# Kernel tuning notes

Hardware: AMD Instinct MI355X
Metric: run time of the kernel (lower is better)

## Reference

```python
import jax, jax.numpy as jnp
import numpy as np

NUM_HEADS = 16  # from init_kwargs


def setup_inputs() -> dict:
    key = jax.random.key(0)
    k1, k2, k3, k4, k5 = jax.random.split(key, 5)
    B, N, C = 2, 2048, 1024
    return {
        "query": jax.random.normal(k1, (B, N, C), dtype=jnp.float32),
        "key": jax.random.normal(k2, (B, N, C), dtype=jnp.float32),
        "value": jax.random.normal(k3, (B, N, C), dtype=jnp.float32),
        "W_merge": jax.random.normal(k4, (C, C), dtype=jnp.float32) * (1.0 / np.sqrt(C)),
        "b_merge": jax.random.normal(k5, (C,), dtype=jnp.float32) * 0.02,
    }


def reference(query, key, value, W_merge, b_merge):
    B, N, C = query.shape
    H = NUM_HEADS
    dim = C // H
    # Faithful to torch: plain reshape (B,N,C) -> (B, dim, H, N), no transpose.
    q = query.reshape(B, dim, H, -1)
    k = key.reshape(B, dim, H, -1)
    v = value.reshape(B, dim, H, -1)
    # Faithful scale: divide by sqrt(N) (sequence length), as in the source.
    scale = 1.0 / np.sqrt(N).astype(np.float32)
    scores = jnp.einsum('bdhn,bdhm->bhnm', q, k) * scale  # [B,H,N,N]
    attn = jax.nn.softmax(scores, axis=-1)
    x = jnp.einsum('bhnm,bdhm->bdhn', attn, v)  # [B,dim,H,N]
    x = x.reshape(B, C, -1)  # [B,C,N]
    # Conv1d(C,C,kernel_size=1) == pointwise channel matmul + bias
    out = jnp.einsum('oc,bcn->bon', W_merge, x) + b_merge[None, :, None]
    return out  # [B,C,N]
```

## Files before the change

### kernel.cpp

```cpp
#include <hip/hip_runtime.h>


#define H 16
#define NSEQ 2048
#define CCH 1024
#define BATCH 2
#define DSTR (H * NSEQ)

typedef __attribute__((ext_vector_type(8))) short bf16x8;
typedef __attribute__((ext_vector_type(4))) float f32x4;
typedef __attribute__((ext_vector_type(16))) float f32x16;
typedef __attribute__((ext_vector_type(4))) unsigned int uint32x4;

__device__ __forceinline__ unsigned short f2bf(float x) {
  unsigned int u = __builtin_bit_cast(unsigned int, x);
  u += 0x7FFFu + ((u >> 16) & 1u);
  return (unsigned short)(u >> 16);
}

__device__ __forceinline__ unsigned int pack2bf(float a, float b) {
#if __has_builtin(__builtin_amdgcn_cvt_pk_bf16_f32)
  typedef __attribute__((ext_vector_type(2))) __bf16 bf16x2_t;
  bf16x2_t r = __builtin_amdgcn_cvt_pk_bf16_f32(a, b);
  return __builtin_bit_cast(unsigned int, r);
#else
  unsigned int ua = __builtin_bit_cast(unsigned int, a);
  unsigned int ub = __builtin_bit_cast(unsigned int, b);
  ua += 0x7FFFu + ((ua >> 16) & 1u);
  ub += 0x7FFFu + ((ub >> 16) & 1u);
  return __builtin_amdgcn_perm(ub, ua, 0x07060302u);
#endif
}

__device__ __forceinline__ float fast_exp2(float x) {
#if __has_builtin(__builtin_amdgcn_exp2f)
  return __builtin_amdgcn_exp2f(x);
#else
  return exp2f(x);
#endif
}

__device__ __forceinline__ void permswap32(unsigned int& a, unsigned int& b) {
#if __has_builtin(__builtin_amdgcn_permlane32_swap)
  typedef __attribute__((ext_vector_type(2))) unsigned int uint2v;
  uint2v r = __builtin_amdgcn_permlane32_swap(a, b, false, false);
  a = r[0];
  b = r[1];
#else
  unsigned int ax = (unsigned int)__shfl_xor((int)a, 32, 64);
  unsigned int bx = (unsigned int)__shfl_xor((int)b, 32, 64);
  bool lo = (threadIdx.x & 63) < 32;
  unsigned int na = lo ? a : bx;
  unsigned int nb = lo ? ax : b;
  a = na;
  b = nb;
#endif
}

__device__ __forceinline__ void gld16(const void* g, void* l) {
  __builtin_amdgcn_global_load_lds(
      (const __attribute__((address_space(1))) unsigned int*)g,
      (__attribute__((address_space(3))) unsigned int*)l, 16, 0, 0);
}

__device__ __forceinline__ f32x16 zero16() {
  f32x16 v;
#pragma unroll
  for (int i = 0; i < 16; ++i) v[i] = 0.f;
  return v;
}

__global__ __launch_bounds__(256) void prep_all(const float* __restrict__ W,
                                                const float* __restrict__ v,
                                                const float* __restrict__ q,
                                                const float* __restrict__ k,
                                                unsigned short* __restrict__ Wp,
                                                unsigned short* __restrict__ Vb,
                                                unsigned short* __restrict__ Qt,
                                                unsigned short* __restrict__ Kt) {
  __shared__ unsigned short T[64][72];
  const int bid = blockIdx.x, tid = threadIdx.x;

  if (bid < 1024) {
    const int o = bid;
    const int cp = tid * 4;
    const int hh = cp >> 6;
    const int d0 = cp & 63;
    const float* Wr = W + (size_t)o * CCH;
    ushort4 ov;
    ov.x = f2bf(Wr[(d0 + 0) * H + hh]);
    ov.y = f2bf(Wr[(d0 + 1) * H + hh]);
    ov.z = f2bf(Wr[(d0 + 2) * H + hh]);
    ov.w = f2bf(Wr[(d0 + 3) * H + hh]);
    *(ushort4*)&Wp[(size_t)o * CCH + cp] = ov;
  } else if (bid < 5120) {
    int idx = (bid - 1024) * 256 + tid;
    float4 x = ((const float4*)v)[idx];
    ushort4 o;
    o.x = f2bf(x.x); o.y = f2bf(x.y); o.z = f2bf(x.z); o.w = f2bf(x.w);
    ((ushort4*)Vb)[idx] = o;
  } else {
    const int lbid = bid - 5120;
    const int n0 = (lbid & 31) * 64;
    const int hh = (lbid >> 5) & 15;
    const int zz = lbid >> 9;
    const int b = zz >> 1, t = zz & 1;
    const float* src = t ? k : q;
    unsigned short* dst = t ? Kt : Qt;
    const float scl = t ? 1.0f : (0.022097086912079608f * 1.4426950408889634f);
    const size_t base = (size_t)b * (CCH * NSEQ) + (size_t)hh * NSEQ;
#pragma unroll
    for (int it = 0; it < 4; ++it) {
      int i4 = it * 256 + tid;
      int d = i4 >> 4;
      int nn = (i4 & 15) << 2;
      float4 val = *(const float4*)(src + base + (size_t)d * DSTR + n0 + nn);
      T[nn + 0][d] = f2bf(val.x * scl);
      T[nn + 1][d] = f2bf(val.y * scl);
      T[nn + 2][d] = f2bf(val.z * scl);
      T[nn + 3][d] = f2bf(val.w * scl);
    }
    __syncthreads();
    const size_t obase = ((size_t)(b * H + hh) * NSEQ + n0) * 64;
#pragma unroll
    for (int it = 0; it < 2; ++it) {
      int idx = it * 256 + tid;
      int row = idx >> 3, cb = idx & 7;
      *(bf16x8*)(dst + obase + (size_t)row * 64 + cb * 8) = *(const bf16x8*)&T[row][cb * 8];
    }
  }
}

__global__ __launch_bounds__(512, 4) void attn6(const unsigned short* __restrict__ Qt,
                                                const unsigned short* __restrict__ Kt,
                                                const unsigned short* __restrict__ Vb,
                                                unsigned short* __restrict__ xt) {
  __shared__ __align__(16) unsigned char sbuf[65536 + 1024];
  unsigned short* KV = (unsigned short*)sbuf;
  float* lsumLDS = (float*)(sbuf + 65536);
  float* Oex = (float*)sbuf;

  const int tid = threadIdx.x;
  const int w = tid >> 6, lane = tid & 63;
  const int lane31 = lane & 31, hl = lane >> 5;
  const int g = w >> 2, nw = w & 3;
  const int n0 = blockIdx.x * 128;
  const int hh = blockIdx.y, b = blockIdx.z;

  const unsigned short* Qbase = Qt + ((size_t)(b * H + hh) * NSEQ + n0) * 64;
  const unsigned short* Kg = Kt + ((size_t)(b * H + hh) * NSEQ + g * 1024) * 64;
  const unsigned short* Vg = Vb + (size_t)b * (CCH * NSEQ) + (size_t)hh * NSEQ + g * 1024;

  const int r8 = lane >> 3, scb = lane & 7;

#define KVOFF(gg, bb, kk) ((((gg)*2 + (bb)) * 2 + (kk)) * 4096)

#pragma unroll
  for (int i = 0; i < 2; ++i) {
    int row = i * 64 + w * 8 + r8;
    int cbl = scb ^ (row & 7);
    gld16(Qbase + (size_t)row * 64 + cbl * 8, KV + (i * 64 + w * 8) * 64);
  }
  __syncthreads();

  bf16x8 bQ[4];
#pragma unroll
  for (int ks = 0; ks < 4; ++ks) {
    int row = nw * 32 + lane31;
    int phys = (ks * 2 + hl) ^ (row & 7);
    bQ[ks] = *(const bf16x8*)(KV + (size_t)row * 64 + phys * 8);
  }
  __syncthreads();

#pragma unroll
  for (int i = 0; i < 2; ++i) {
    int row = i * 32 + nw * 8 + r8;
    int cbl = scb ^ (row & 7);
    gld16(Kg + (size_t)row * 64 + cbl * 8, KV + KVOFF(g, 0, 0) + (i * 32 + nw * 8) * 64);
    gld16(Vg + (size_t)row * DSTR + cbl * 8, KV + KVOFF(g, 0, 1) + (i * 32 + nw * 8) * 64);
  }
  __syncthreads();

  f32x16 O[2];
  O[0] = zero16();
  O[1] = zero16();
  float lsum = 0.f;

  for (int it = 0; it < 16; ++it) {
    const int cur = it & 1;
    if (it < 15) {
      const int nxt = cur ^ 1;
      const int m0n = (it + 1) * 64;
#pragma unroll
      for (int i = 0; i < 2; ++i) {
        int row = i * 32 + nw * 8 + r8;
        int cbl = scb ^ (row & 7);
        gld16(Kg + (size_t)(m0n + row) * 64 + cbl * 8,
              KV + KVOFF(g, nxt, 0) + (i * 32 + nw * 8) * 64);
        gld16(Vg + (size_t)row * DSTR + m0n + cbl * 8,
              KV + KVOFF(g, nxt, 1) + (i * 32 + nw * 8) * 64);
      }
    }

#pragma unroll
    for (int mt = 0; mt < 2; ++mt) {
      f32x16 St = zero16();
#pragma unroll
      for (int ks = 0; ks < 4; ++ks) {
        int row = mt * 32 + lane31;
        int phys = (ks * 2 + hl) ^ (row & 7);
        bf16x8 aK = *(const bf16x8*)(KV + KVOFF(g, cur, 0) + row * 64 + phys * 8);
        St = __builtin_amdgcn_mfma_f32_32x32x16_bf16(aK, bQ[ks], St, 0, 0, 0);
      }

      unsigned int pd[8];
#pragma unroll
      for (int t = 0; t < 8; ++t) {
        float e0 = fast_exp2(St[2 * t]);
        float e1 = fast_exp2(St[2 * t + 1]);
        lsum += e0 + e1;
        pd[t] = pack2bf(e0, e1);
      }

      unsigned int s0[4] = {pd[0], pd[1], pd[2], pd[3]};
      unsigned int s1[4] = {pd[4], pd[5], pd[6], pd[7]};
      permswap32(s0[0], s0[2]);
      permswap32(s0[1], s0[3]);
      permswap32(s1[0], s1[2]);
      permswap32(s1[1], s1[3]);

#pragma unroll
      for (int ms = 0; ms < 2; ++ms) {
        bf16x8 bV[2];
#pragma unroll
        for (int dt = 0; dt < 2; ++dt) {
          int row = dt * 32 + lane31;
          int phys = (mt * 4 + ms * 2 + hl) ^ (row & 7);
          bV[dt] = *(const bf16x8*)(KV + KVOFF(g, cur, 1) + row * 64 + phys * 8);
        }
        const unsigned int* sp = ms ? s1 : s0;
        bf16x8 aP = __builtin_bit_cast(bf16x8, (uint32x4){sp[0], sp[1], sp[2], sp[3]});
        O[0] = __builtin_amdgcn_mfma_f32_32x32x16_bf16(aP, bV[0], O[0], 0, 0, 0);
        O[1] = __builtin_amdgcn_mfma_f32_32x32x16_bf16(aP, bV[1], O[1], 0, 0, 0);
      }
    }
    __syncthreads();
  }

  lsum += __shfl_xor(lsum, 32, 64);
  if (hl == 0) lsumLDS[g * 128 + nw * 32 + lane31] = lsum;
  if (g == 1) {
#pragma unroll
    for (int dt = 0; dt < 2; ++dt)
#pragma unroll
      for (int r = 0; r < 16; ++r) {
        int nl = nw * 32 + (r & 3) + 8 * (r >> 2) + 4 * hl;
        Oex[nl * 64 + dt * 32 + lane31] = O[dt][r];
      }
  }
  __syncthreads();
  if (g == 0) {
    const size_t xb = (size_t)b * ((size_t)NSEQ * CCH);
#pragma unroll
    for (int rq = 0; rq < 4; ++rq) {
      int nlb = nw * 32 + rq * 8 + 4 * hl;
      float4 l0 = *(const float4*)&lsumLDS[nlb];
      float4 l1 = *(const float4*)&lsumLDS[128 + nlb];
      float inv0 = 1.0f / (l0.x + l1.x);
      float inv1 = 1.0f / (l0.y + l1.y);
      float inv2 = 1.0f / (l0.z + l1.z);
      float inv3 = 1.0f / (l0.w + l1.w);
#pragma unroll
      for (int dt = 0; dt < 2; ++dt) {
        int d = dt * 32 + lane31;
#pragma unroll
        for (int rr = 0; rr < 4; ++rr) {
          int r = rq * 4 + rr;
          float val = O[dt][r] + Oex[(nlb + rr) * 64 + d];
          float inv = (rr == 0) ? inv0 : (rr == 1) ? inv1 : (rr == 2) ? inv2 : inv3;
          int n = n0 + nlb + rr;
          xt[xb + (size_t)n * CCH + hh * 64 + d] = f2bf(val * inv);
        }
      }
    }
  }
#undef KVOFF
}

__global__ __launch_bounds__(256) void merge5(const unsigned short* __restrict__ Wp,
                                              const unsigned short* __restrict__ xt,
                                              const float* __restrict__ bias,
                                              float* __restrict__ out) {
  __shared__ unsigned short At[2][64 * 64];
  __shared__ unsigned short Bt[2][64 * 64];
  const int tid = threadIdx.x;
  const int w = tid >> 6, lane = tid & 63;
  const int quad = lane >> 4, l16 = lane & 15;
  const int wx = w & 1, wy = w >> 1;
  const int n0 = blockIdx.x * 64, o0 = blockIdx.y * 64, b = blockIdx.z;
  const int srow = w * 8 + (lane >> 3), scb = lane & 7;
  const unsigned short* Bbase = xt + (size_t)b * ((size_t)NSEQ * CCH);

  f32x4 acc[2][2];
#pragma unroll
  for (int ot = 0; ot < 2; ++ot)
#pragma unroll
    for (int nt = 0; nt < 2; ++nt) acc[ot][nt] = (f32x4){0.f, 0.f, 0.f, 0.f};

#pragma unroll
  for (int i = 0; i < 2; ++i) {
    int row = i * 32 + srow;
    int cbl = scb ^ (row & 7);
    gld16(Wp + (size_t)(o0 + row) * CCH + cbl * 8, &At[0][(i * 32 + w * 8) * 64]);
    gld16(Bbase + (size_t)(n0 + row) * CCH + cbl * 8, &Bt[0][(i * 32 + w * 8) * 64]);
  }
  __syncthreads();

  for (int it = 0; it < 16; ++it) {
    const int cur = it & 1;
    if (it < 15) {
      const int nxt = cur ^ 1;
      const int c0 = (it + 1) * 64;
#pragma unroll
      for (int i = 0; i < 2; ++i) {
        int row = i * 32 + srow;
        int cbl = scb ^ (row & 7);
        gld16(Wp + (size_t)(o0 + row) * CCH + c0 + cbl * 8, &At[nxt][(i * 32 + w * 8) * 64]);
        gld16(Bbase + (size_t)(n0 + row) * CCH + c0 + cbl * 8, &Bt[nxt][(i * 32 + w * 8) * 64]);
      }
    }
#pragma unroll
    for (int ks = 0; ks < 2; ++ks) {
      int phys = ((ks * 4 + quad) ^ (l16 & 7)) * 8;
      bf16x8 aW[2], bX[2];
#pragma unroll
      for (int ot = 0; ot < 2; ++ot)
        aW[ot] = *(const bf16x8*)&At[cur][(wy * 32 + ot * 16 + l16) * 64 + phys];
#pragma unroll
      for (int nt = 0; nt < 2; ++nt)
        bX[nt] = *(const bf16x8*)&Bt[cur][(wx * 32 + nt * 16 + l16) * 64 + phys];
#pragma unroll
      for (int ot = 0; ot < 2; ++ot)
#pragma unroll
        for (int nt = 0; nt < 2; ++nt)
          acc[ot][nt] =
              __builtin_amdgcn_mfma_f32_16x16x32_bf16(aW[ot], bX[nt], acc[ot][nt], 0, 0, 0);
    }
    __syncthreads();
  }

#pragma unroll
  for (int ot = 0; ot < 2; ++ot) {
#pragma unroll
    for (int r = 0; r < 4; ++r) {
      int o = o0 + wy * 32 + ot * 16 + quad * 4 + r;
      float br = bias[o];
#pragma unroll
      for (int nt = 0; nt < 2; ++nt)
        out[(size_t)b * ((size_t)CCH * NSEQ) + (size_t)o * NSEQ + n0 + wx * 32 + nt * 16 + l16] =
            acc[ot][nt][r] + br;
    }
  }
}

extern "C" void kernel_launch(void* const* d_in, const int* in_sizes, int n_in,
                              void* d_out, int out_size, void* d_ws, size_t ws_size,
                              hipStream_t stream) {
  const float* q = (const float*)d_in[0];
  const float* k = (const float*)d_in[1];
  const float* v = (const float*)d_in[2];
  const float* W = (const float*)d_in[3];
  const float* bias = (const float*)d_in[4];
  float* out = (float*)d_out;

  unsigned short* Wp = (unsigned short*)d_ws;
  unsigned short* xt = Wp + (1u << 20);
  unsigned short* Qt = xt + (4u << 20);
  unsigned short* Kt = Qt + (4u << 20);
  unsigned short* Vb = Kt + (4u << 20);

  hipLaunchKernelGGL(prep_all, dim3(7168), dim3(256), 0, stream, W, v, q, k, Wp, Vb, Qt, Kt);
  hipLaunchKernelGGL(attn6, dim3(NSEQ / 128, H, BATCH), dim3(512), 0, stream, Qt, Kt, Vb, xt);
  hipLaunchKernelGGL(merge5, dim3(NSEQ / 64, CCH / 64, BATCH), dim3(256), 0, stream,
                     Wp, xt, bias, out);
}
```

Before: 162.4 us.

## Software-pipeline QK MFMA ahead of softmax and change LDS swizzle

Restructures the attention inner loop so the QK^T tile for the next sub-block is issued before the exp/pack and PV MFMAs of the current one. This includes computing the first tile of the next iteration right after the barrier. The goal is to overlap MFMA latency with the VALU exp work. It also widens the LDS XOR swizzle to mix in row bits 3-4, reducing bank conflicts, and splits the row-sum into two accumulators to shorten the dependency chain. An extra live f32x16 accumulator raises register pressure, which could hurt occupancy.

```diff
diff --git a/kernel.cpp b/kernel.cpp
--- a/kernel.cpp
+++ b/kernel.cpp
@@ -8,6 +8,7 @@
 #define DSTR (H * NSEQ)
 
 typedef __attribute__((ext_vector_type(8))) short bf16x8;
+typedef __attribute__((ext_vector_type(2))) float f32x2;
 typedef __attribute__((ext_vector_type(4))) float f32x4;
 typedef __attribute__((ext_vector_type(16))) float f32x16;
 typedef __attribute__((ext_vector_type(4))) unsigned int uint32x4;
@@ -69,6 +70,8 @@
   for (int i = 0; i < 16; ++i) v[i] = 0.f;
   return v;
 }
+
+__device__ __forceinline__ int swzr(int row) { return (row & 7) ^ ((row >> 3) & 3); }
 
 __global__ __launch_bounds__(256) void prep_all(const float* __restrict__ W,
                                                 const float* __restrict__ v,
@@ -131,7 +134,60 @@
   }
 }
 
-__global__ __launch_bounds__(512, 4) void attn6(const unsigned short* __restrict__ Qt,
+
+__device__ __forceinline__ f32x16 qk_tile(const unsigned short* Kt, int mt, int lane31,
+                                          int hl, const bf16x8* bQ) {
+  const int row = mt * 32 + lane31;
+  const int s = swzr(row);
+  const unsigned short* rp = Kt + (size_t)row * 64;
+  f32x16 St = zero16();
+#pragma unroll
+  for (int ks = 0; ks < 4; ++ks) {
+    bf16x8 aK = *(const bf16x8*)(rp + (((ks * 2 + hl) ^ s) * 8));
+    St = __builtin_amdgcn_mfma_f32_32x32x16_bf16(aK, bQ[ks], St, 0, 0, 0);
+  }
+  return St;
+}
+
+__device__ __forceinline__ void exppack(const f32x16& St, f32x2& ls2, bf16x8& a0, bf16x8& a1) {
+  unsigned int pd[8];
+#pragma unroll
+  for (int t = 0; t < 8; ++t) {
+    float e0 = fast_exp2(St[2 * t]);
+    float e1 = fast_exp2(St[2 * t + 1]);
+    ls2 += (f32x2){e0, e1};
+    pd[t] = pack2bf(e0, e1);
+  }
+  unsigned int s0[4] = {pd[0], pd[1], pd[2], pd[3]};
+  unsigned int s1[4] = {pd[4], pd[5], pd[6], pd[7]};
+  permswap32(s0[0], s0[2]);
+  permswap32(s0[1], s0[3]);
+  permswap32(s1[0], s1[2]);
+  permswap32(s1[1], s1[3]);
+  a0 = __builtin_bit_cast(bf16x8, (uint32x4){s0[0], s0[1], s0[2], s0[3]});
+  a1 = __builtin_bit_cast(bf16x8, (uint32x4){s1[0], s1[1], s1[2], s1[3]});
+}
+
+__device__ __forceinline__ void pv_tile(const unsigned short* Vt, int mt, bf16x8 a0, bf16x8 a1,
+                                        int lane31, int hl, f32x16& O0, f32x16& O1) {
+#pragma unroll
+  for (int ms = 0; ms < 2; ++ms) {
+    bf16x8 bV0, bV1;
+    {
+      int row = lane31;
+      bV0 = *(const bf16x8*)(Vt + (size_t)row * 64 + (((mt * 4 + ms * 2 + hl) ^ swzr(row)) * 8));
+    }
+    {
+      int row = 32 + lane31;
+      bV1 = *(const bf16x8*)(Vt + (size_t)row * 64 + (((mt * 4 + ms * 2 + hl) ^ swzr(row)) * 8));
+    }
+    bf16x8 aP = ms ? a1 : a0;
+    O0 = __builtin_amdgcn_mfma_f32_32x32x16_bf16(aP, bV0, O0, 0, 0, 0);
+    O1 = __builtin_amdgcn_mfma_f32_32x32x16_bf16(aP, bV1, O1, 0, 0, 0);
+  }
+}
+
+__global__ __launch_bounds__(512, 4) void attn7(const unsigned short* __restrict__ Qt,
                                                 const unsigned short* __restrict__ Kt,
                                                 const unsigned short* __restrict__ Vb,
                                                 unsigned short* __restrict__ xt) {
@@ -158,7 +214,7 @@
 #pragma unroll
   for (int i = 0; i < 2; ++i) {
     int row = i * 64 + w * 8 + r8;
-    int cbl = scb ^ (row & 7);
+    int cbl = scb ^ swzr(row);
     gld16(Qbase + (size_t)row * 64 + cbl * 8, KV + (i * 64 + w * 8) * 64);
   }
   __syncthreads();
@@ -167,7 +223,7 @@
 #pragma unroll
   for (int ks = 0; ks < 4; ++ks) {
     int row = nw * 32 + lane31;
-    int phys = (ks * 2 + hl) ^ (row & 7);
+    int phys = (ks * 2 + hl) ^ swzr(row);
     bQ[ks] = *(const bf16x8*)(KV + (size_t)row * 64 + phys * 8);
   }
   __syncthreads();
@@ -175,7 +231,7 @@
 #pragma unroll
   for (int i = 0; i < 2; ++i) {
     int row = i * 32 + nw * 8 + r8;
-    int cbl = scb ^ (row & 7);
+    int cbl = scb ^ swzr(row);
     gld16(Kg + (size_t)row * 64 + cbl * 8, KV + KVOFF(g, 0, 0) + (i * 32 + nw * 8) * 64);
     gld16(Vg + (size_t)row * DSTR + cbl * 8, KV + KVOFF(g, 0, 1) + (i * 32 + nw * 8) * 64);
   }
@@ -184,7 +240,9 @@
   f32x16 O[2];
   O[0] = zero16();
   O[1] = zero16();
-  float lsum = 0.f;
+  f32x2 ls2 = {0.f, 0.f};
+
+  f32x16 St0 = qk_tile(KV + KVOFF(g, 0, 0), 0, lane31, hl, bQ);
 
   for (int it = 0; it < 16; ++it) {
     const int cur = it & 1;
@@ -194,7 +252,7 @@
 #pragma unroll
       for (int i = 0; i < 2; ++i) {
         int row = i * 32 + nw * 8 + r8;
-        int cbl = scb ^ (row & 7);
+        int cbl = scb ^ swzr(row);
         gld16(Kg + (size_t)(m0n + row) * 64 + cbl * 8,
               KV + KVOFF(g, nxt, 0) + (i * 32 + nw * 8) * 64);
         gld16(Vg + (size_t)row * DSTR + m0n + cbl * 8,
@@ -202,51 +260,23 @@
       }
     }
 
-#pragma unroll
-    for (int mt = 0; mt < 2; ++mt) {
-      f32x16 St = zero16();
-#pragma unroll
-      for (int ks = 0; ks < 4; ++ks) {
-        int row = mt * 32 + lane31;
-        int phys = (ks * 2 + hl) ^ (row & 7);
-        bf16x8 aK = *(const bf16x8*)(KV + KVOFF(g, cur, 0) + row * 64 + phys * 8);
-        St = __builtin_amdgcn_mfma_f32_32x32x16_bf16(aK, bQ[ks], St, 0, 0, 0);
-      }
-
-      unsigned int pd[8];
-#pragma unroll
-      for (int t = 0; t < 8; ++t) {
-        float e0 = fast_exp2(St[2 * t]);
-        float e1 = fast_exp2(St[2 * t + 1]);
-        lsum += e0 + e1;
-        pd[t] = pack2bf(e0, e1);
-      }
-
-      unsigned int s0[4] = {pd[0], pd[1], pd[2], pd[3]};
-      unsigned int s1[4] = {pd[4], pd[5], pd[6], pd[7]};
-      permswap32(s0[0], s0[2]);
-      permswap32(s0[1], s0[3]);
-      permswap32(s1[0], s1[2]);
-      permswap32(s1[1], s1[3]);
-
-#pragma unroll
-      for (int ms = 0; ms < 2; ++ms) {
-        bf16x8 bV[2];
-#pragma unroll
-        for (int dt = 0; dt < 2; ++dt) {
-          int row = dt * 32 + lane31;
-          int phys = (mt * 4 + ms * 2 + hl) ^ (row & 7);
-          bV[dt] = *(const bf16x8*)(KV + KVOFF(g, cur, 1) + row * 64 + phys * 8);
-        }
-        const unsigned int* sp = ms ? s1 : s0;
-        bf16x8 aP = __builtin_bit_cast(bf16x8, (uint32x4){sp[0], sp[1], sp[2], sp[3]});
-        O[0] = __builtin_amdgcn_mfma_f32_32x32x16_bf16(aP, bV[0], O[0], 0, 0, 0);
-        O[1] = __builtin_amdgcn_mfma_f32_32x32x16_bf16(aP, bV[1], O[1], 0, 0, 0);
-      }
-    }
+    const unsigned short* Ktile = KV + KVOFF(g, cur, 0);
+    const unsigned short* Vtile = KV + KVOFF(g, cur, 1);
+
+    f32x16 St1 = qk_tile(Ktile, 1, lane31, hl, bQ);
+
+    bf16x8 a0, a1;
+    exppack(St0, ls2, a0, a1);
+    pv_tile(Vtile, 0, a0, a1, lane31, hl, O[0], O[1]);
+
+    exppack(St1, ls2, a0, a1);
+    pv_tile(Vtile, 1, a0, a1, lane31, hl, O[0], O[1]);
+
     __syncthreads();
-  }
-
+    if (it < 15) St0 = qk_tile(KV + KVOFF(g, cur ^ 1, 0), 0, lane31, hl, bQ);
+  }
+
+  float lsum = ls2[0] + ls2[1];
   lsum += __shfl_xor(lsum, 32, 64);
   if (hl == 0) lsumLDS[g * 128 + nw * 32 + lane31] = lsum;
   if (g == 1) {
@@ -380,7 +410,7 @@
   unsigned short* Vb = Kt + (4u << 20);
 
   hipLaunchKernelGGL(prep_all, dim3(7168), dim3(256), 0, stream, W, v, q, k, Wp, Vb, Qt, Kt);
-  hipLaunchKernelGGL(attn6, dim3(NSEQ / 128, H, BATCH), dim3(512), 0, stream, Qt, Kt, Vb, xt);
+  hipLaunchKernelGGL(attn7, dim3(NSEQ / 128, H, BATCH), dim3(512), 0, stream, Qt, Kt, Vb, xt);
   hipLaunchKernelGGL(merge5, dim3(NSEQ / 64, CCH / 64, BATCH), dim3(256), 0, stream,
                      Wp, xt, bias, out);
 }
```

Result: no change. 162.8 us (+0.3%).

## Restructure attention inner loop with unrolled double buffering, precomputed LDS pointers, and setprio

Applied to the files above, without the earlier changes.

Rewrites the attention kernel's main loop into a manually unrolled two-stage ping-pong, with LDS read pointers and global staging pointers precomputed outside the loop. It also changes the LDS swizzle to XOR in extra row bits, to reduce bank conflicts. MFMA sections are bracketed with s_setprio so matrix work gets issue priority over the exp and pack work, and the row sum is kept as a two-wide vector to shorten the dependency chain. The aim is to cut address arithmetic and conflicts and to improve overlap. The cost is more complex code and possible register pressure, and the new swizzle has to stay consistent with the layout used in the epilogue.

```diff
diff --git a/kernel.cpp b/kernel.cpp
--- a/kernel.cpp
+++ b/kernel.cpp
@@ -8,6 +8,7 @@
 #define DSTR (H * NSEQ)
 
 typedef __attribute__((ext_vector_type(8))) short bf16x8;
+typedef __attribute__((ext_vector_type(2))) float f32x2;
 typedef __attribute__((ext_vector_type(4))) float f32x4;
 typedef __attribute__((ext_vector_type(16))) float f32x16;
 typedef __attribute__((ext_vector_type(4))) unsigned int uint32x4;
@@ -69,6 +70,8 @@
   for (int i = 0; i < 16; ++i) v[i] = 0.f;
   return v;
 }
+
+__device__ __forceinline__ int swzr(int row) { return (row & 7) ^ ((row >> 3) & 3); }
 
 __global__ __launch_bounds__(256) void prep_all(const float* __restrict__ W,
                                                 const float* __restrict__ v,
@@ -131,7 +134,37 @@
   }
 }
 
-__global__ __launch_bounds__(512, 4) void attn6(const unsigned short* __restrict__ Qt,
+
+__device__ __forceinline__ f32x16 qk4(const char* const* kp, int off, const bf16x8* bQ) {
+  f32x16 St = zero16();
+#pragma unroll
+  for (int ks = 0; ks < 4; ++ks) {
+    bf16x8 aK = *(const bf16x8*)(kp[ks] + off);
+    St = __builtin_amdgcn_mfma_f32_32x32x16_bf16(aK, bQ[ks], St, 0, 0, 0);
+  }
+  return St;
+}
+
+__device__ __forceinline__ void exppack(const f32x16& St, f32x2& ls2, bf16x8& a0, bf16x8& a1) {
+  unsigned int pd[8];
+#pragma unroll
+  for (int t = 0; t < 8; ++t) {
+    float e0 = fast_exp2(St[2 * t]);
+    float e1 = fast_exp2(St[2 * t + 1]);
+    ls2 += (f32x2){e0, e1};
+    pd[t] = pack2bf(e0, e1);
+  }
+  unsigned int s0[4] = {pd[0], pd[1], pd[2], pd[3]};
+  unsigned int s1[4] = {pd[4], pd[5], pd[6], pd[7]};
+  permswap32(s0[0], s0[2]);
+  permswap32(s0[1], s0[3]);
+  permswap32(s1[0], s1[2]);
+  permswap32(s1[1], s1[3]);
+  a0 = __builtin_bit_cast(bf16x8, (uint32x4){s0[0], s0[1], s0[2], s0[3]});
+  a1 = __builtin_bit_cast(bf16x8, (uint32x4){s1[0], s1[1], s1[2], s1[3]});
+}
+
+__global__ __launch_bounds__(512, 4) void attn8(const unsigned short* __restrict__ Qt,
                                                 const unsigned short* __restrict__ Kt,
                                                 const unsigned short* __restrict__ Vb,
                                                 unsigned short* __restrict__ xt) {
@@ -158,7 +191,7 @@
 #pragma unroll
   for (int i = 0; i < 2; ++i) {
     int row = i * 64 + w * 8 + r8;
-    int cbl = scb ^ (row & 7);
+    int cbl = scb ^ swzr(row);
     gld16(Qbase + (size_t)row * 64 + cbl * 8, KV + (i * 64 + w * 8) * 64);
   }
   __syncthreads();
@@ -167,86 +200,98 @@
 #pragma unroll
   for (int ks = 0; ks < 4; ++ks) {
     int row = nw * 32 + lane31;
-    int phys = (ks * 2 + hl) ^ (row & 7);
+    int phys = (ks * 2 + hl) ^ swzr(row);
     bQ[ks] = *(const bf16x8*)(KV + (size_t)row * 64 + phys * 8);
   }
   __syncthreads();
 
-#pragma unroll
-  for (int i = 0; i < 2; ++i) {
-    int row = i * 32 + nw * 8 + r8;
-    int cbl = scb ^ (row & 7);
-    gld16(Kg + (size_t)row * 64 + cbl * 8, KV + KVOFF(g, 0, 0) + (i * 32 + nw * 8) * 64);
-    gld16(Vg + (size_t)row * DSTR + cbl * 8, KV + KVOFF(g, 0, 1) + (i * 32 + nw * 8) * 64);
-  }
+  const char* KVc = (const char*)KV;
+  const int sz = swzr(lane31);
+  const char* kp[4];
+#pragma unroll
+  for (int ks = 0; ks < 4; ++ks)
+    kp[ks] = KVc + g * 32768 + lane31 * 128 + (((ks * 2 + hl) ^ sz) * 16);
+
+  const int srow0 = nw * 8 + r8;
+  const int cswz = (scb ^ swzr(srow0)) * 16;
+  const char* kgp0 = (const char*)Kg + (size_t)srow0 * 128 + cswz;
+  const char* kgp1 = kgp0 + 4096;
+  const char* vgp0 = (const char*)Vg + (size_t)srow0 * (DSTR * 2) + cswz;
+  const char* vgp1 = vgp0 + (size_t)32 * DSTR * 2;
+
+  unsigned short* ldsK0 = KV + KVOFF(g, 0, 0) + (nw * 8) * 64;
+  unsigned short* ldsK1 = ldsK0 + 32 * 64;
+  unsigned short* ldsV0 = KV + KVOFF(g, 0, 1) + (nw * 8) * 64;
+  unsigned short* ldsV1 = ldsV0 + 32 * 64;
+
+  gld16(kgp0, ldsK0);
+  gld16(kgp1, ldsK1);
+  gld16(vgp0, ldsV0);
+  gld16(vgp1, ldsV1);
+  kgp0 += 8192; kgp1 += 8192; vgp0 += 128; vgp1 += 128;
   __syncthreads();
 
   f32x16 O[2];
   O[0] = zero16();
   O[1] = zero16();
-  float lsum = 0.f;
-
-  for (int it = 0; it < 16; ++it) {
-    const int cur = it & 1;
-    if (it < 15) {
-      const int nxt = cur ^ 1;
-      const int m0n = (it + 1) * 64;
-#pragma unroll
-      for (int i = 0; i < 2; ++i) {
-        int row = i * 32 + nw * 8 + r8;
-        int cbl = scb ^ (row & 7);
-        gld16(Kg + (size_t)(m0n + row) * 64 + cbl * 8,
-              KV + KVOFF(g, nxt, 0) + (i * 32 + nw * 8) * 64);
-        gld16(Vg + (size_t)row * DSTR + m0n + cbl * 8,
-              KV + KVOFF(g, nxt, 1) + (i * 32 + nw * 8) * 64);
-      }
-    }
-
-#pragma unroll
-    for (int mt = 0; mt < 2; ++mt) {
-      f32x16 St = zero16();
-#pragma unroll
-      for (int ks = 0; ks < 4; ++ks) {
-        int row = mt * 32 + lane31;
-        int phys = (ks * 2 + hl) ^ (row & 7);
-        bf16x8 aK = *(const bf16x8*)(KV + KVOFF(g, cur, 0) + row * 64 + phys * 8);
-        St = __builtin_amdgcn_mfma_f32_32x32x16_bf16(aK, bQ[ks], St, 0, 0, 0);
-      }
-
-      unsigned int pd[8];
-#pragma unroll
-      for (int t = 0; t < 8; ++t) {
-        float e0 = fast_exp2(St[2 * t]);
-        float e1 = fast_exp2(St[2 * t + 1]);
-        lsum += e0 + e1;
-        pd[t] = pack2bf(e0, e1);
-      }
-
-      unsigned int s0[4] = {pd[0], pd[1], pd[2], pd[3]};
-      unsigned int s1[4] = {pd[4], pd[5], pd[6], pd[7]};
-      permswap32(s0[0], s0[2]);
-      permswap32(s0[1], s0[3]);
-      permswap32(s1[0], s1[2]);
-      permswap32(s1[1], s1[3]);
-
-#pragma unroll
-      for (int ms = 0; ms < 2; ++ms) {
-        bf16x8 bV[2];
-#pragma unroll
-        for (int dt = 0; dt < 2; ++dt) {
-          int row = dt * 32 + lane31;
-          int phys = (mt * 4 + ms * 2 + hl) ^ (row & 7);
-          bV[dt] = *(const bf16x8*)(KV + KVOFF(g, cur, 1) + row * 64 + phys * 8);
-        }
-        const unsigned int* sp = ms ? s1 : s0;
-        bf16x8 aP = __builtin_bit_cast(bf16x8, (uint32x4){sp[0], sp[1], sp[2], sp[3]});
-        O[0] = __builtin_amdgcn_mfma_f32_32x32x16_bf16(aP, bV[0], O[0], 0, 0, 0);
-        O[1] = __builtin_amdgcn_mfma_f32_32x32x16_bf16(aP, bV[1], O[1], 0, 0, 0);
-      }
-    }
-    __syncthreads();
-  }
-
+  f32x2 ls2 = {0.f, 0.f};
+
+#define VREAD(C, DT, CUR) (*(const bf16x8*)(kp[C] + 8192 + (DT)*4096 + (CUR)*16384))
+
+#define PVT(MT, CUR, A0, A1)                                                     \
+  {                                                                              \
+    bf16x8 v00 = VREAD((MT)*2 + 0, 0, CUR);                                      \
+    bf16x8 v01 = VREAD((MT)*2 + 0, 1, CUR);                                      \
+    bf16x8 v10 = VREAD((MT)*2 + 1, 0, CUR);                                      \
+    bf16x8 v11 = VREAD((MT)*2 + 1, 1, CUR);                                      \
+    O[0] = __builtin_amdgcn_mfma_f32_32x32x16_bf16(A0, v00, O[0], 0, 0, 0);      \
+    O[1] = __builtin_amdgcn_mfma_f32_32x32x16_bf16(A0, v01, O[1], 0, 0, 0);      \
+    O[0] = __builtin_amdgcn_mfma_f32_32x32x16_bf16(A1, v10, O[0], 0, 0, 0);      \
+    O[1] = __builtin_amdgcn_mfma_f32_32x32x16_bf16(A1, v11, O[1], 0, 0, 0);      \
+  }
+
+#define ATTN_ITER(CUR, DO_STAGE)                                                 \
+  {                                                                              \
+    if (DO_STAGE) {                                                              \
+      gld16(kgp0, ldsK0 + (1 - (CUR)) * 8192);                                   \
+      gld16(kgp1, ldsK1 + (1 - (CUR)) * 8192);                                   \
+      gld16(vgp0, ldsV0 + (1 - (CUR)) * 8192);                                   \
+      gld16(vgp1, ldsV1 + (1 - (CUR)) * 8192);                                   \
+      kgp0 += 8192; kgp1 += 8192; vgp0 += 128; vgp1 += 128;                      \
+    }                                                                            \
+    {                                                                            \
+      __builtin_amdgcn_s_setprio(1);                                             \
+      f32x16 St = qk4(kp, (CUR)*16384, bQ);                                      \
+      __builtin_amdgcn_s_setprio(0);                                             \
+      bf16x8 a0, a1;                                                             \
+      exppack(St, ls2, a0, a1);                                                  \
+      __builtin_amdgcn_s_setprio(1);                                             \
+      PVT(0, CUR, a0, a1);                                                       \
+      __builtin_amdgcn_s_setprio(0);                                             \
+    }                                                                            \
+    {                                                                            \
+      __builtin_amdgcn_s_setprio(1);                                             \
+      f32x16 St = qk4(kp, 4096 + (CUR)*16384, bQ);                               \
+      __builtin_amdgcn_s_setprio(0);                                             \
+      bf16x8 a0, a1;                                                             \
+      exppack(St, ls2, a0, a1);                                                  \
+      __builtin_amdgcn_s_setprio(1);                                             \
+      PVT(1, CUR, a0, a1);                                                       \
+      __builtin_amdgcn_s_setprio(0);                                             \
+    }                                                                            \
+    __syncthreads();                                                             \
+  }
+
+  for (int j = 0; j < 8; ++j) {
+    ATTN_ITER(0, 1);
+    ATTN_ITER(1, (j < 7));
+  }
+
+#undef ATTN_ITER
+#undef PVT
+#undef VREAD
+
+  float lsum = ls2[0] + ls2[1];
   lsum += __shfl_xor(lsum, 32, 64);
   if (hl == 0) lsumLDS[g * 128 + nw * 32 + lane31] = lsum;
   if (g == 1) {
@@ -380,7 +425,7 @@
   unsigned short* Vb = Kt + (4u << 20);
 
   hipLaunchKernelGGL(prep_all, dim3(7168), dim3(256), 0, stream, W, v, q, k, Wp, Vb, Qt, Kt);
-  hipLaunchKernelGGL(attn6, dim3(NSEQ / 128, H, BATCH), dim3(512), 0, stream, Qt, Kt, Vb, xt);
+  hipLaunchKernelGGL(attn8, dim3(NSEQ / 128, H, BATCH), dim3(512), 0, stream, Qt, Kt, Vb, xt);
   hipLaunchKernelGGL(merge5, dim3(NSEQ / 64, CCH / 64, BATCH), dim3(256), 0, stream,
                      Wp, xt, bias, out);
 }
```

Result: slower. 167.6 us (+3.2%).

## Pre-swizzle K and V into MFMA fragment order and load directly from global

Applied to the files above, without the earlier changes.

The prep kernel now writes K and V in a layout that matches the MFMA operand fragments, with V transposed through shared memory. The attention kernel then drops its LDS double buffering and per-tile block barriers, and loads K/V fragments straight from global memory with register double buffering. It also adds s_setprio around the MFMA groups. This removes LDS traffic and synchronisation, but relies on L2/cache hits for K/V reuse across waves and issues many small global loads.

```diff
diff --git a/kernel.cpp b/kernel.cpp
--- a/kernel.cpp
+++ b/kernel.cpp
@@ -8,6 +8,7 @@
 #define DSTR (H * NSEQ)
 
 typedef __attribute__((ext_vector_type(8))) short bf16x8;
+typedef __attribute__((ext_vector_type(2))) float f32x2;
 typedef __attribute__((ext_vector_type(4))) float f32x4;
 typedef __attribute__((ext_vector_type(16))) float f32x16;
 typedef __attribute__((ext_vector_type(4))) unsigned int uint32x4;
@@ -75,10 +76,11 @@
                                                 const float* __restrict__ q,
                                                 const float* __restrict__ k,
                                                 unsigned short* __restrict__ Wp,
-                                                unsigned short* __restrict__ Vb,
+                                                unsigned short* __restrict__ VB,
                                                 unsigned short* __restrict__ Qt,
-                                                unsigned short* __restrict__ Kt) {
+                                                unsigned short* __restrict__ KA) {
   __shared__ unsigned short T[64][72];
+  __shared__ unsigned short VL[256 * 8];
   const int bid = blockIdx.x, tid = threadIdx.x;
 
   if (bid < 1024) {
@@ -93,20 +95,29 @@
     ov.z = f2bf(Wr[(d0 + 2) * H + hh]);
     ov.w = f2bf(Wr[(d0 + 3) * H + hh]);
     *(ushort4*)&Wp[(size_t)o * CCH + cp] = ov;
-  } else if (bid < 5120) {
-    int idx = (bid - 1024) * 256 + tid;
-    float4 x = ((const float4*)v)[idx];
-    ushort4 o;
-    o.x = f2bf(x.x); o.y = f2bf(x.y); o.z = f2bf(x.z); o.w = f2bf(x.w);
-    ((ushort4*)Vb)[idx] = o;
+  } else if (bid < 3072) {
+    const int vb = bid - 1024;
+    const int bh = vb >> 6, kbb = vb & 63;
+    const int bb = bh >> 4, hhh = bh & 15;
+    const int d = tid >> 2, nq = (tid & 3) * 8;
+    const float* srcv =
+        v + (size_t)bb * (CCH * NSEQ) + (size_t)d * DSTR + hhh * NSEQ + kbb * 32 + nq;
+    float4 x0 = *(const float4*)srcv;
+    float4 x1 = *(const float4*)(srcv + 4);
+    unsigned short* Lc = &VL[tid * 8];
+    Lc[0] = f2bf(x0.x); Lc[1] = f2bf(x0.y); Lc[2] = f2bf(x0.z); Lc[3] = f2bf(x0.w);
+    Lc[4] = f2bf(x1.x); Lc[5] = f2bf(x1.y); Lc[6] = f2bf(x1.z); Lc[7] = f2bf(x1.w);
+    __syncthreads();
+    const int kb_lo = tid >> 6, d2 = tid & 63;
+    *(bf16x8*)(VB + (size_t)bh * 131072 + (size_t)(kbb * 4 + kb_lo) * 512 + d2 * 8) =
+        *(const bf16x8*)&VL[(d2 * 4 + kb_lo) * 8];
   } else {
-    const int lbid = bid - 5120;
+    const int lbid = bid - 3072;
     const int n0 = (lbid & 31) * 64;
     const int hh = (lbid >> 5) & 15;
     const int zz = lbid >> 9;
     const int b = zz >> 1, t = zz & 1;
     const float* src = t ? k : q;
-    unsigned short* dst = t ? Kt : Qt;
     const float scl = t ? 1.0f : (0.022097086912079608f * 1.4426950408889634f);
     const size_t base = (size_t)b * (CCH * NSEQ) + (size_t)hh * NSEQ;
 #pragma unroll
@@ -121,24 +132,54 @@
       T[nn + 3][d] = f2bf(val.w * scl);
     }
     __syncthreads();
-    const size_t obase = ((size_t)(b * H + hh) * NSEQ + n0) * 64;
-#pragma unroll
-    for (int it = 0; it < 2; ++it) {
-      int idx = it * 256 + tid;
-      int row = idx >> 3, cb = idx & 7;
-      *(bf16x8*)(dst + obase + (size_t)row * 64 + cb * 8) = *(const bf16x8*)&T[row][cb * 8];
-    }
-  }
-}
-
-__global__ __launch_bounds__(512, 4) void attn6(const unsigned short* __restrict__ Qt,
-                                                const unsigned short* __restrict__ Kt,
-                                                const unsigned short* __restrict__ Vb,
+    if (t == 0) {
+      const size_t obase = ((size_t)(b * H + hh) * NSEQ + n0) * 64;
+#pragma unroll
+      for (int it = 0; it < 2; ++it) {
+        int idx = it * 256 + tid;
+        int row = idx >> 3, cb = idx & 7;
+        *(bf16x8*)(Qt + obase + (size_t)row * 64 + cb * 8) = *(const bf16x8*)&T[row][cb * 8];
+      }
+    } else {
+      const size_t obase = (size_t)(b * H + hh) * 131072 + (size_t)(n0 >> 5) * 2048;
+#pragma unroll
+      for (int it = 0; it < 2; ++it) {
+        int idx = it * 256 + tid;
+        int nl = idx >> 3, sub = idx & 7;
+        *(bf16x8*)(KA + obase + (size_t)(nl >> 5) * 2048 + sub * 256 + (nl & 31) * 8) =
+            *(const bf16x8*)&T[nl][sub * 8];
+      }
+    }
+  }
+}
+
+
+__device__ __forceinline__ void exppack(const f32x16& St, f32x2& ls2, bf16x8& a0, bf16x8& a1) {
+  unsigned int pd[8];
+#pragma unroll
+  for (int t = 0; t < 8; ++t) {
+    float e0 = fast_exp2(St[2 * t]);
+    float e1 = fast_exp2(St[2 * t + 1]);
+    ls2 += (f32x2){e0, e1};
+    pd[t] = pack2bf(e0, e1);
+  }
+  unsigned int s0[4] = {pd[0], pd[1], pd[2], pd[3]};
+  unsigned int s1[4] = {pd[4], pd[5], pd[6], pd[7]};
+  permswap32(s0[0], s0[2]);
+  permswap32(s0[1], s0[3]);
+  permswap32(s1[0], s1[2]);
+  permswap32(s1[1], s1[3]);
+  a0 = __builtin_bit_cast(bf16x8, (uint32x4){s0[0], s0[1], s0[2], s0[3]});
+  a1 = __builtin_bit_cast(bf16x8, (uint32x4){s1[0], s1[1], s1[2], s1[3]});
+}
+
+__global__ __launch_bounds__(512, 4) void attn9(const unsigned short* __restrict__ Qt,
+                                                const unsigned short* __restrict__ KA,
+                                                const unsigned short* __restrict__ VB,
                                                 unsigned short* __restrict__ xt) {
-  __shared__ __align__(16) unsigned char sbuf[65536 + 1024];
-  unsigned short* KV = (unsigned short*)sbuf;
-  float* lsumLDS = (float*)(sbuf + 65536);
-  float* Oex = (float*)sbuf;
+  __shared__ __align__(16) float eplds[128 * 64 + 256];
+  float* Oex = eplds;
+  float* lsumLDS = eplds + 8192;
 
   const int tid = threadIdx.x;
   const int w = tid >> 6, lane = tid & 63;
@@ -146,107 +187,67 @@
   const int g = w >> 2, nw = w & 3;
   const int n0 = blockIdx.x * 128;
   const int hh = blockIdx.y, b = blockIdx.z;
-
-  const unsigned short* Qbase = Qt + ((size_t)(b * H + hh) * NSEQ + n0) * 64;
-  const unsigned short* Kg = Kt + ((size_t)(b * H + hh) * NSEQ + g * 1024) * 64;
-  const unsigned short* Vg = Vb + (size_t)b * (CCH * NSEQ) + (size_t)hh * NSEQ + g * 1024;
-
-  const int r8 = lane >> 3, scb = lane & 7;
-
-#define KVOFF(gg, bb, kk) ((((gg)*2 + (bb)) * 2 + (kk)) * 4096)
-
-#pragma unroll
-  for (int i = 0; i < 2; ++i) {
-    int row = i * 64 + w * 8 + r8;
-    int cbl = scb ^ (row & 7);
-    gld16(Qbase + (size_t)row * 64 + cbl * 8, KV + (i * 64 + w * 8) * 64);
-  }
-  __syncthreads();
+  const int bh = b * H + hh;
 
   bf16x8 bQ[4];
-#pragma unroll
-  for (int ks = 0; ks < 4; ++ks) {
-    int row = nw * 32 + lane31;
-    int phys = (ks * 2 + hl) ^ (row & 7);
-    bQ[ks] = *(const bf16x8*)(KV + (size_t)row * 64 + phys * 8);
-  }
-  __syncthreads();
-
-#pragma unroll
-  for (int i = 0; i < 2; ++i) {
-    int row = i * 32 + nw * 8 + r8;
-    int cbl = scb ^ (row & 7);
-    gld16(Kg + (size_t)row * 64 + cbl * 8, KV + KVOFF(g, 0, 0) + (i * 32 + nw * 8) * 64);
-    gld16(Vg + (size_t)row * DSTR + cbl * 8, KV + KVOFF(g, 0, 1) + (i * 32 + nw * 8) * 64);
-  }
-  __syncthreads();
+  const unsigned short* Qb = Qt + ((size_t)bh * NSEQ + n0 + nw * 32 + lane31) * 64;
+#pragma unroll
+  for (int ks = 0; ks < 4; ++ks) bQ[ks] = *(const bf16x8*)(Qb + (ks * 2 + hl) * 8);
+
+  const unsigned short* kp = KA + (size_t)bh * 131072 + g * 65536 + hl * 256 + lane31 * 8;
+  const unsigned short* vp = VB + (size_t)bh * 131072 + g * 65536 + hl * 512 + lane31 * 8;
 
   f32x16 O[2];
   O[0] = zero16();
   O[1] = zero16();
-  float lsum = 0.f;
-
-  for (int it = 0; it < 16; ++it) {
-    const int cur = it & 1;
-    if (it < 15) {
-      const int nxt = cur ^ 1;
-      const int m0n = (it + 1) * 64;
-#pragma unroll
-      for (int i = 0; i < 2; ++i) {
-        int row = i * 32 + nw * 8 + r8;
-        int cbl = scb ^ (row & 7);
-        gld16(Kg + (size_t)(m0n + row) * 64 + cbl * 8,
-              KV + KVOFF(g, nxt, 0) + (i * 32 + nw * 8) * 64);
-        gld16(Vg + (size_t)row * DSTR + m0n + cbl * 8,
-              KV + KVOFF(g, nxt, 1) + (i * 32 + nw * 8) * 64);
-      }
-    }
-
-#pragma unroll
-    for (int mt = 0; mt < 2; ++mt) {
-      f32x16 St = zero16();
-#pragma unroll
-      for (int ks = 0; ks < 4; ++ks) {
-        int row = mt * 32 + lane31;
-        int phys = (ks * 2 + hl) ^ (row & 7);
-        bf16x8 aK = *(const bf16x8*)(KV + KVOFF(g, cur, 0) + row * 64 + phys * 8);
-        St = __builtin_amdgcn_mfma_f32_32x32x16_bf16(aK, bQ[ks], St, 0, 0, 0);
-      }
-
-      unsigned int pd[8];
-#pragma unroll
-      for (int t = 0; t < 8; ++t) {
-        float e0 = fast_exp2(St[2 * t]);
-        float e1 = fast_exp2(St[2 * t + 1]);
-        lsum += e0 + e1;
-        pd[t] = pack2bf(e0, e1);
-      }
-
-      unsigned int s0[4] = {pd[0], pd[1], pd[2], pd[3]};
-      unsigned int s1[4] = {pd[4], pd[5], pd[6], pd[7]};
-      permswap32(s0[0], s0[2]);
-      permswap32(s0[1], s0[3]);
-      permswap32(s1[0], s1[2]);
-      permswap32(s1[1], s1[3]);
-
-#pragma unroll
-      for (int ms = 0; ms < 2; ++ms) {
-        bf16x8 bV[2];
-#pragma unroll
-        for (int dt = 0; dt < 2; ++dt) {
-          int row = dt * 32 + lane31;
-          int phys = (mt * 4 + ms * 2 + hl) ^ (row & 7);
-          bV[dt] = *(const bf16x8*)(KV + KVOFF(g, cur, 1) + row * 64 + phys * 8);
-        }
-        const unsigned int* sp = ms ? s1 : s0;
-        bf16x8 aP = __builtin_bit_cast(bf16x8, (uint32x4){sp[0], sp[1], sp[2], sp[3]});
-        O[0] = __builtin_amdgcn_mfma_f32_32x32x16_bf16(aP, bV[0], O[0], 0, 0, 0);
-        O[1] = __builtin_amdgcn_mfma_f32_32x32x16_bf16(aP, bV[1], O[1], 0, 0, 0);
-      }
-    }
-    __syncthreads();
-  }
-
+  f32x2 ls2 = {0.f, 0.f};
+
+#define LOADK(R0, R1, R2, R3, C)                      \
+  {                                                   \
+    const unsigned short* kc_ = kp + (C)*2048;        \
+    R0 = *(const bf16x8*)(kc_);                       \
+    R1 = *(const bf16x8*)(kc_ + 512);                 \
+    R2 = *(const bf16x8*)(kc_ + 1024);                \
+    R3 = *(const bf16x8*)(kc_ + 1536);                \
+  }
+
+#define CHUNK(K0, K1, K2, K3, C)                                                \
+  {                                                                             \
+    __builtin_amdgcn_s_setprio(1);                                              \
+    f32x16 St = zero16();                                                       \
+    St = __builtin_amdgcn_mfma_f32_32x32x16_bf16(K0, bQ[0], St, 0, 0, 0);       \
+    St = __builtin_amdgcn_mfma_f32_32x32x16_bf16(K1, bQ[1], St, 0, 0, 0);       \
+    St = __builtin_amdgcn_mfma_f32_32x32x16_bf16(K2, bQ[2], St, 0, 0, 0);       \
+    St = __builtin_amdgcn_mfma_f32_32x32x16_bf16(K3, bQ[3], St, 0, 0, 0);       \
+    __builtin_amdgcn_s_setprio(0);                                              \
+    bf16x8 a0, a1;                                                              \
+    exppack(St, ls2, a0, a1);                                                   \
+    const unsigned short* vc_ = vp + (C)*2048;                                  \
+    bf16x8 v00 = *(const bf16x8*)(vc_);                                         \
+    bf16x8 v01 = *(const bf16x8*)(vc_ + 256);                                   \
+    bf16x8 v10 = *(const bf16x8*)(vc_ + 1024);                                  \
+    bf16x8 v11 = *(const bf16x8*)(vc_ + 1280);                                  \
+    __builtin_amdgcn_s_setprio(1);                                              \
+    O[0] = __builtin_amdgcn_mfma_f32_32x32x16_bf16(a0, v00, O[0], 0, 0, 0);     \
+    O[1] = __builtin_amdgcn_mfma_f32_32x32x16_bf16(a0, v01, O[1], 0, 0, 0);     \
+    O[0] = __builtin_amdgcn_mfma_f32_32x32x16_bf16(a1, v10, O[0], 0, 0, 0);     \
+    O[1] = __builtin_amdgcn_mfma_f32_32x32x16_bf16(a1, v11, O[1], 0, 0, 0);     \
+    __builtin_amdgcn_s_setprio(0);                                              \
+  }
+
+  bf16x8 kA0, kA1, kA2, kA3, kB0, kB1, kB2, kB3;
+  LOADK(kA0, kA1, kA2, kA3, 0);
+  for (int j = 0; j < 16; ++j) {
+    LOADK(kB0, kB1, kB2, kB3, 2 * j + 1);
+    CHUNK(kA0, kA1, kA2, kA3, 2 * j);
+    LOADK(kA0, kA1, kA2, kA3, 2 * j + 2);
+    CHUNK(kB0, kB1, kB2, kB3, 2 * j + 1);
+    if ((j & 3) == 3) __syncthreads();
+  }
+#undef CHUNK
+#undef LOADK
+
+  float lsum = ls2[0] + ls2[1];
   lsum += __shfl_xor(lsum, 32, 64);
   if (hl == 0) lsumLDS[g * 128 + nw * 32 + lane31] = lsum;
   if (g == 1) {
@@ -284,7 +285,6 @@
       }
     }
   }
-#undef KVOFF
 }
 
 __global__ __launch_bounds__(256) void merge5(const unsigned short* __restrict__ Wp,
@@ -376,11 +376,11 @@
   unsigned short* Wp = (unsigned short*)d_ws;
   unsigned short* xt = Wp + (1u << 20);
   unsigned short* Qt = xt + (4u << 20);
-  unsigned short* Kt = Qt + (4u << 20);
-  unsigned short* Vb = Kt + (4u << 20);
-
-  hipLaunchKernelGGL(prep_all, dim3(7168), dim3(256), 0, stream, W, v, q, k, Wp, Vb, Qt, Kt);
-  hipLaunchKernelGGL(attn6, dim3(NSEQ / 128, H, BATCH), dim3(512), 0, stream, Qt, Kt, Vb, xt);
+  unsigned short* KA = Qt + (4u << 20);
+  unsigned short* VB = KA + (4u << 20);
+
+  hipLaunchKernelGGL(prep_all, dim3(5120), dim3(256), 0, stream, W, v, q, k, Wp, VB, Qt, KA);
+  hipLaunchKernelGGL(attn9, dim3(NSEQ / 128, H, BATCH), dim3(512), 0, stream, Qt, KA, VB, xt);
   hipLaunchKernelGGL(merge5, dim3(NSEQ / 64, CCH / 64, BATCH), dim3(256), 0, stream,
                      Wp, xt, bias, out);
 }
```

Result: no change. 162.6 us (+0.2%).
